# Kernel tuning notes

Measured on AMD Instinct MI355X. Metric: run time of the kernel, lower is better.

The kernel has to match this reference:

```python
import jax, jax.numpy as jnp
import numpy as np

MEM, KEY, VAL, DIN, BS, BQ = 1000, 64, 128, 512, 512, 65536


def setup_inputs() -> dict:
    key = jax.random.key(0)
    ks = jax.random.split(key, 20)

    def lin(k, fan_in, shape):
        return (jax.random.normal(k, shape, jnp.float32) / np.sqrt(fan_in)).astype(jnp.float32)

    return {
        "support_x": jax.random.normal(ks[0], (BS, DIN), jnp.float32),
        "support_y": jax.random.normal(ks[1], (BS, VAL), jnp.float32),
        "query_x": jax.random.normal(ks[2], (BQ, DIN), jnp.float32),
        "query_y": jax.random.normal(ks[3], (BQ, 1), jnp.float32),
        # base model: Linear(DIN -> KEY)
        "base_W": lin(ks[4], DIN, (DIN, KEY)),
        "base_b": jnp.zeros((KEY,), jnp.float32),
        # ExternalMemory projections
        "kp_W": lin(ks[5], KEY, (KEY, KEY)),
        "kp_b": jnp.zeros((KEY,), jnp.float32),
        "vp_W": lin(ks[6], VAL, (VAL, VAL)),
        "vp_b": jnp.zeros((VAL,), jnp.float32),
        # memory buffers (randn keys/values like register_buffer(torch.randn))
        "mem_keys": jax.random.normal(ks[7], (MEM, KEY), jnp.float32),
        "mem_values": jax.random.normal(ks[8], (MEM, VAL), jnp.float32),
        # ages: uniform so top-k picks distinct slots deterministically
        "mem_age": jax.random.uniform(ks[9], (MEM,), jnp.float32),
        # controller MLP: Linear(KEY+VAL,128) ReLU Linear(128,64) ReLU Linear(64,1)
        "c1_W": lin(ks[10], KEY + VAL, (KEY + VAL, 128)),
        "c1_b": jnp.zeros((128,), jnp.float32),
        "c2_W": lin(ks[11], 128, (128, 64)),
        "c2_b": jnp.zeros((64,), jnp.float32),
        "c3_W": lin(ks[12], 64, (64, 1)),
        "c3_b": jnp.zeros((1,), jnp.float32),
    }


def reference(support_x, support_y, query_x, query_y,
              base_W, base_b, kp_W, kp_b, vp_W, vp_b,
              mem_keys, mem_values, mem_age,
              c1_W, c1_b, c2_W, c2_b, c3_W, c3_b):
    # base model features
    support_feat = support_x @ base_W + base_b          # [BS, KEY]
    query_feat = query_x @ base_W + base_b              # [BQ, KEY]

    # --- memory.write(support_feat, support_y) ---
    proj_keys = support_feat @ kp_W + kp_b              # [BS, KEY]
    proj_vals = support_y @ vp_W + vp_b                 # [BS, VAL]
    _, oldest = jax.lax.top_k(mem_age, BS)              # evict oldest BS slots
    new_keys = mem_keys.at[oldest].set(proj_keys)       # [MEM, KEY]
    new_values = mem_values.at[oldest].set(proj_vals)   # [MEM, VAL]

    # --- memory.read(query_feat) ---
    proj_q = query_feat @ kp_W + kp_b                   # [BQ, KEY]
    sims = proj_q @ new_keys.T                          # [BQ, MEM]
    attn = jax.nn.softmax(sims, axis=-1)
    retrieved = attn @ new_values                       # [BQ, VAL]

    # --- controller MLP on [query_feat ; retrieved] ---
    aug = jnp.concatenate([query_feat, retrieved], axis=-1)  # [BQ, KEY+VAL]
    h = jax.nn.relu(aug @ c1_W + c1_b)
    h = jax.nn.relu(h @ c2_W + c2_b)
    query_pred = h @ c3_W + c3_b                        # [BQ, 1]

    meta_loss = jnp.mean((query_pred - query_y) ** 2)
    return meta_loss, query_pred, retrieved
```

## Files before the change

### kernel.cpp

```cpp
#include <hip/hip_runtime.h>

typedef _Float16 h8v __attribute__((ext_vector_type(8)));
typedef _Float16 h4v __attribute__((ext_vector_type(4)));
typedef float    f4v __attribute__((ext_vector_type(4)));

#define MFMA16(a,b,c) __builtin_amdgcn_mfma_f32_16x16x32_f16((a),(b),(c),0,0,0)
#define NEGF (-1e30f)

#define MEM 1000
#define KEY 64
#define VAL 128
#define DIN 512
#define BS  512
#define BQ  65536


typedef __attribute__((address_space(1))) const unsigned int guint;
typedef __attribute__((address_space(3))) unsigned int luint;

__device__ __forceinline__ void gld16(const _Float16* g, _Float16* l)
{
  __builtin_amdgcn_global_load_lds((guint*)g, (luint*)l, 16, 0, 0);
}

__device__ __forceinline__ h8v cvt8(const float* p)
{
  f4v u = *(const f4v*)p;
  f4v v = *(const f4v*)(p + 4);
  h8v a;
  a[0] = (_Float16)u.x; a[1] = (_Float16)u.y; a[2] = (_Float16)u.z; a[3] = (_Float16)u.w;
  a[4] = (_Float16)v.x; a[5] = (_Float16)v.y; a[6] = (_Float16)v.z; a[7] = (_Float16)v.w;
  return a;
}

__device__ __forceinline__ h8v cvt8nt(const float* p)
{
  f4v u = __builtin_nontemporal_load((const f4v*)p);
  f4v v = __builtin_nontemporal_load((const f4v*)(p + 4));
  h8v a;
  a[0] = (_Float16)u.x; a[1] = (_Float16)u.y; a[2] = (_Float16)u.z; a[3] = (_Float16)u.w;
  a[4] = (_Float16)v.x; a[5] = (_Float16)v.y; a[6] = (_Float16)v.z; a[7] = (_Float16)v.w;
  return a;
}

__global__ void k_prep1(const float* __restrict__ baseW, const float* __restrict__ base_b,
                        const float* __restrict__ kpW, const float* __restrict__ kp_b,
                        const float* __restrict__ vpW, const float* __restrict__ c1W,
                        const float* __restrict__ c2W, const float* __restrict__ age,
                        _Float16* __restrict__ WTf, float* __restrict__ bcomb,
                        _Float16* __restrict__ vpWt, _Float16* __restrict__ c1F,
                        _Float16* __restrict__ c2F, int* __restrict__ ranks,
                        float* __restrict__ out0)
{
  long id = (long)blockIdx.x * 256 + threadIdx.x;
  if (id < 65536) {
    int h = (int)id;
    int j = h & 7, lane = (h >> 3) & 63, KS = (h >> 9) & 15, F = h >> 13;
    int n = F * 16 + (lane & 15);
    int k = KS * 32 + ((lane >> 4) << 3) + j;
    float v;
    if (n < 64) v = baseW[(size_t)k * 64 + n];
    else {
      int nn = n - 64;
      const float* br = baseW + (size_t)k * 64;
      float s = 0.f;
      for (int t = 0; t < 64; ++t) s += br[t] * kpW[t * 64 + nn];
      v = s;
    }
    WTf[h] = (_Float16)v;
  } else if (id < 65664) {
    int i = (int)(id - 65536);
    if (i < 64) bcomb[i] = base_b[i];
    else {
      int n = i - 64;
      float s = kp_b[n];
      for (int t = 0; t < 64; ++t) s += base_b[t] * kpW[t * 64 + n];
      bcomb[i] = s;
    }
  } else if (id < 90240) {
    int h = (int)(id - 65664);
    int j = h & 7, lane = (h >> 3) & 63, KS = (h >> 9) % 6, F = (h >> 9) / 6;
    int n = F * 16 + (lane & 15);
    int k = KS * 32 + ((lane >> 4) << 3) + j;
    c1F[h] = (_Float16)c1W[(size_t)k * 128 + n];
  } else if (id < 98432) {
    int h = (int)(id - 90240);
    int j = h & 7, lane = (h >> 3) & 63, KS = (h >> 9) & 3, F = h >> 11;
    int n = F * 16 + (lane & 15);
    int k = KS * 32 + ((lane >> 4) << 3) + j;
    c2F[h] = (_Float16)c2W[(size_t)k * 64 + n];
  } else if (id < 114816) {
    long i = id - 98432;
    int n = (int)(i >> 7), k = (int)(i & 127);
    vpWt[i] = (_Float16)vpW[(size_t)k * 128 + n];
  } else if (id < 115816) {
    int jx = (int)(id - 114816);
    float aj = age[jx];
    int r = 0;
    for (int i2 = 0; i2 < MEM; ++i2) {
      float ai = age[i2];
      r += (ai > aj) || (ai == aj && i2 < jx);
    }
    ranks[jx] = r;
  } else if (id == 115816) {
    *out0 = 0.f;
  }
}

__global__ __launch_bounds__(64) void k_prep2(
    const float* __restrict__ sx, const float* __restrict__ sy,
    const _Float16* __restrict__ WTf, const float* __restrict__ bcomb,
    const _Float16* __restrict__ vpWt, const float* __restrict__ vp_b,
    float* __restrict__ pkeys, float* __restrict__ pvals)
{
  const int lane = threadIdx.x, quad = lane >> 4, l15 = lane & 15;
  const f4v fz = {0.f, 0.f, 0.f, 0.f};
  if (blockIdx.x < 32) {
    const int m0 = blockIdx.x * 16;
    f4v acc[4];
    #pragma unroll
    for (int f = 0; f < 4; ++f) acc[f] = fz;
    const float* xr = sx + (size_t)(m0 + l15) * DIN;
    #pragma unroll 4
    for (int ks = 0; ks < 16; ++ks) {
      int k0 = ks * 32 + quad * 8;
      h8v a = cvt8(xr + k0);
      #pragma unroll
      for (int f = 0; f < 4; ++f) {
        h8v b = *(const h8v*)(WTf + (size_t)((((4 + f) * 16) + ks) * 64 + lane) * 8);
        acc[f] = MFMA16(a, b, acc[f]);
      }
    }
    #pragma unroll
    for (int f = 0; f < 4; ++f) {
      int col = f * 16 + l15;
      float bb = bcomb[64 + col];
      #pragma unroll
      for (int r = 0; r < 4; ++r)
        pkeys[(size_t)(m0 + quad * 4 + r) * KEY + col] = acc[f][r] + bb;
    }
  } else {
    const int m0 = (blockIdx.x - 32) * 16;
    f4v acc[8];
    #pragma unroll
    for (int f = 0; f < 8; ++f) acc[f] = fz;
    const float* yr = sy + (size_t)(m0 + l15) * VAL;
    #pragma unroll
    for (int ks = 0; ks < 4; ++ks) {
      int k0 = ks * 32 + quad * 8;
      h8v a = cvt8(yr + k0);
      #pragma unroll
      for (int f = 0; f < 8; ++f) {
        h8v b = *(const h8v*)(vpWt + (size_t)(f * 16 + l15) * 128 + k0);
        acc[f] = MFMA16(a, b, acc[f]);
      }
    }
    #pragma unroll
    for (int f = 0; f < 8; ++f) {
      int col = f * 16 + l15;
      float bb = vp_b[col];
      #pragma unroll
      for (int r = 0; r < 4; ++r)
        pvals[(size_t)(m0 + quad * 4 + r) * VAL + col] = acc[f][r] + bb;
    }
  }
}

__global__ void k_prep3(const int* __restrict__ ranks, const float* __restrict__ pk,
                        const float* __restrict__ pv, const float* __restrict__ memK,
                        const float* __restrict__ memV,
                        _Float16* __restrict__ keysF, _Float16* __restrict__ valF)
{
  int id = blockIdx.x * 256 + threadIdx.x;
  if (id < 65536) {
    int j = id & 7, lane = (id >> 3) & 63, KS = (id >> 9) & 1, F = id >> 10;
    int n = F * 16 + (lane & 15);
    int k = KS * 32 + ((lane >> 4) << 3) + j;
    float v = 0.f;
    if (n < MEM) {
      int rk = ranks[n];
      v = (rk < BS) ? pk[(size_t)rk * KEY + k] : memK[(size_t)n * KEY + k];
    }
    keysF[id] = (_Float16)v;
  } else {
    int h = id - 65536;
    int j = h & 7, lane = (h >> 3) & 63, KS = (h >> 9) & 31, F = h >> 14;
    int nv = F * 16 + (lane & 15);
    int jm = KS * 32 + ((lane >> 4) << 3) + j;
    float v = 0.f;
    if (jm < MEM) {
      int rk = ranks[jm];
      v = (rk < BS) ? pv[(size_t)rk * VAL + nv] : memV[(size_t)jm * VAL + nv];
    }
    valF[h] = (_Float16)v;
  }
}

__global__ __launch_bounds__(512) void k_feat(const float* __restrict__ qx,
                                              const _Float16* __restrict__ WTf,
                                              const float* __restrict__ bcomb,
                                              _Float16* __restrict__ qfpq)
{
  __shared__ __align__(16) _Float16 WTsh[65536];

  const int tid = threadIdx.x, wid = tid >> 6, lane = tid & 63;
  const int quad = lane >> 4, l15 = lane & 15;

  #pragma unroll
  for (int i = 0; i < 16; ++i) {
    const int t = wid * 16 + i;
    gld16(WTf + (size_t)t * 512 + lane * 8, WTsh + t * 512);
  }
  asm volatile("s_waitcnt vmcnt(0)" ::: "memory");
  __syncthreads();

  const int tile = blockIdx.x * 8 + wid;
  const int q0 = tile * 16;
  const f4v fz = {0.f, 0.f, 0.f, 0.f};
  f4v acc[8];
  #pragma unroll
  for (int f = 0; f < 8; ++f) acc[f] = fz;

  const float* xr = qx + (size_t)(q0 + l15) * DIN;

  #pragma unroll 4
  for (int ks = 0; ks < 16; ++ks) {
    const int k0 = ks * 32 + quad * 8;
    h8v a = cvt8nt(xr + k0);
    #pragma unroll
    for (int f = 0; f < 8; ++f) {
      h8v b = *(const h8v*)(WTsh + (size_t)((f * 16 + ks) * 64 + lane) * 8);
      acc[f] = MFMA16(a, b, acc[f]);
    }
  }

  __syncthreads();
  _Float16* tbuf = WTsh + wid * 2176;

  #pragma unroll
  for (int f = 0; f < 8; ++f) {
    float bb = bcomb[f * 16 + l15];
    #pragma unroll
    for (int r = 0; r < 4; ++r)
      tbuf[(quad * 4 + r) * 136 + f * 16 + l15] = (_Float16)(acc[f][r] + bb);
  }
  const size_t ob = (size_t)tile * 4 * 512;
  #pragma unroll
  for (int KS = 0; KS < 4; ++KS) {
    h8v v = *(const h8v*)&tbuf[l15 * 136 + KS * 32 + quad * 8];
    __builtin_nontemporal_store(v, (h8v*)(qfpq + ob + KS * 512 + lane * 8));
  }
}

__global__ __launch_bounds__(512) void k_main(
    const _Float16* __restrict__ qfpq, const float* __restrict__ qy,
    const float* __restrict__ c1_b, const float* __restrict__ c2_b,
    const float* __restrict__ c3W, const float* __restrict__ c3b,
    const _Float16* __restrict__ c1F, const _Float16* __restrict__ c2F,
    const _Float16* __restrict__ keysF, const _Float16* __restrict__ valF,
    float* __restrict__ dout)
{
  __shared__ __align__(16) _Float16 Ksh[2][8192];
  __shared__ __align__(16) _Float16 Vsh[2][16384];
  __shared__ __align__(16) _Float16 Pwk[8][3328];

  const int tid  = threadIdx.x;
  const int wid  = tid >> 6;
  const int lane = tid & 63;
  const int quad = lane >> 4;
  const int l15  = lane & 15;
  const int tile = blockIdx.x * 8 + wid;
  const int q0   = tile * 16;

  _Float16* P_s  = Pwk[wid];
  _Float16* h2_s = Pwk[wid] + 2176;

  float* out_pred = dout + 1;
  float* out_ret  = dout + 1 + BQ;
  const f4v fz = {0.f, 0.f, 0.f, 0.f};

  {
    const _Float16* kc = keysF;
    #pragma unroll
    for (int i = 0; i < 2; ++i) {
      const int t = wid * 2 + i;
      gld16(kc + (size_t)t * 512 + lane * 8, Ksh[0] + t * 512);
    }
    #pragma unroll
    for (int i = 0; i < 4; ++i) {
      const int t = wid * 4 + i;
      const int v = t >> 2, sub = t & 3;
      gld16(valF + ((size_t)(v * 32 + 0 * 4 + sub)) * 512 + lane * 8,
            Vsh[0] + (v * 4 + sub) * 512);
    }
  }

  const size_t fb = (size_t)tile * 4 * 512;
  h8v pq0 = __builtin_nontemporal_load((const h8v*)(qfpq + fb + 2 * 512 + lane * 8));
  h8v pq1 = __builtin_nontemporal_load((const h8v*)(qfpq + fb + 3 * 512 + lane * 8));

  asm volatile("s_waitcnt vmcnt(0)" ::: "memory");
  __syncthreads();

  float rm[4], rl[4];
  #pragma unroll
  for (int r = 0; r < 4; ++r) { rm[r] = NEGF; rl[r] = 0.f; }
  f4v O[8];
  #pragma unroll
  for (int v = 0; v < 8; ++v) O[v] = fz;

  #pragma unroll 1
  for (int c = 0; c < 8; ++c) {
    const int cur = c & 1;

    if (c < 7) {
      const int nc = c + 1;
      const _Float16* kc = keysF + (size_t)nc * 8192;
      #pragma unroll
      for (int i = 0; i < 2; ++i) {
        const int t = wid * 2 + i;
        gld16(kc + (size_t)t * 512 + lane * 8, Ksh[cur ^ 1] + t * 512);
      }
      #pragma unroll
      for (int i = 0; i < 4; ++i) {
        const int t = wid * 4 + i;
        const int v = t >> 2, sub = t & 3;
        gld16(valF + ((size_t)(v * 32 + nc * 4 + sub)) * 512 + lane * 8,
              Vsh[cur ^ 1] + (v * 4 + sub) * 512);
      }
    }

    f4v S[8];
    #pragma unroll
    for (int f = 0; f < 8; ++f) S[f] = fz;
    const _Float16* Kb = Ksh[cur];
    #pragma unroll
    for (int f = 0; f < 8; ++f) {
      h8v b0 = *(const h8v*)(Kb + (size_t)(f * 2 + 0) * 512 + lane * 8);
      h8v b1 = *(const h8v*)(Kb + (size_t)(f * 2 + 1) * 512 + lane * 8);
      S[f] = MFMA16(pq0, b0, S[f]);
      S[f] = MFMA16(pq1, b1, S[f]);
    }

    float cm[4] = {NEGF, NEGF, NEGF, NEGF};
    #pragma unroll
    for (int f = 0; f < 8; ++f) {
      const int col = c * 128 + f * 16 + l15;
      const bool ok = (col < MEM);
      #pragma unroll
      for (int r = 0; r < 4; ++r) {
        float s = ok ? S[f][r] : NEGF;
        S[f][r] = s;
        cm[r] = fmaxf(cm[r], s);
      }
    }
    #pragma unroll
    for (int r = 0; r < 4; ++r) {
      #pragma unroll
      for (int m = 1; m < 16; m <<= 1) cm[r] = fmaxf(cm[r], __shfl_xor(cm[r], m));
    }
    float al[4];
    #pragma unroll
    for (int r = 0; r < 4; ++r) {
      float mn = fmaxf(rm[r], cm[r]);
      al[r] = __expf(rm[r] - mn);
      rm[r] = mn;
    }
    float psl[4] = {0.f, 0.f, 0.f, 0.f};
    #pragma unroll
    for (int f = 0; f < 8; ++f)
      #pragma unroll
      for (int r = 0; r < 4; ++r) {
        float p = __expf(S[f][r] - rm[r]);
        S[f][r] = p;
        psl[r] += p;
      }
    #pragma unroll
    for (int r = 0; r < 4; ++r) rl[r] = rl[r] * al[r] + psl[r];

    #pragma unroll
    for (int f = 0; f < 8; ++f)
      #pragma unroll
      for (int r = 0; r < 4; ++r)
        P_s[(quad * 4 + r) * 136 + f * 16 + l15] = (_Float16)S[f][r];
    #pragma unroll
    for (int v = 0; v < 8; ++v)
      #pragma unroll
      for (int r = 0; r < 4; ++r) O[v][r] *= al[r];
    const _Float16* Vb = Vsh[cur];
    #pragma unroll
    for (int ks = 0; ks < 4; ++ks) {
      h8v a = *(const h8v*)&P_s[l15 * 136 + ks * 32 + quad * 8];
      #pragma unroll
      for (int v = 0; v < 8; ++v) {
        h8v b = *(const h8v*)(Vb + (size_t)(v * 4 + ks) * 512 + lane * 8);
        O[v] = MFMA16(a, b, O[v]);
      }
    }

    asm volatile("s_waitcnt vmcnt(0)" ::: "memory");
    __syncthreads();
  }

  #pragma unroll
  for (int r = 0; r < 4; ++r) {
    #pragma unroll
    for (int m = 1; m < 16; m <<= 1) rl[r] += __shfl_xor(rl[r], m);
  }

  #pragma unroll
  for (int v = 0; v < 8; ++v)
    #pragma unroll
    for (int r = 0; r < 4; ++r)
      P_s[(quad * 4 + r) * 136 + v * 16 + l15] = (_Float16)(O[v][r] / rl[r]);

  #pragma unroll
  for (int it = 0; it < 8; ++it) {
    int flat = it * 256 + lane * 4;
    int row = flat >> 7, col = flat & 127;
    h4v t = *(const h4v*)&P_s[row * 136 + col];
    f4v o;
    o.x = (float)t[0]; o.y = (float)t[1]; o.z = (float)t[2]; o.w = (float)t[3];
    __builtin_nontemporal_store(o, (f4v*)(out_ret + (size_t)q0 * VAL + flat));
  }

  h8v qf0 = __builtin_nontemporal_load((const h8v*)(qfpq + fb + 0 * 512 + lane * 8));
  h8v qf1 = __builtin_nontemporal_load((const h8v*)(qfpq + fb + 1 * 512 + lane * 8));
  {
    f4v H[8];
    #pragma unroll
    for (int f = 0; f < 8; ++f) H[f] = fz;
    #pragma unroll
    for (int ks = 0; ks < 6; ++ks) {
      const int k0 = ks * 32;
      h8v a = (ks == 0) ? qf0 : (ks == 1) ? qf1
               : *(const h8v*)&P_s[l15 * 136 + (k0 - 64) + quad * 8];
      #pragma unroll
      for (int f = 0; f < 8; ++f) {
        h8v b = *(const h8v*)(c1F + (size_t)(f * 6 + ks) * 512 + lane * 8);
        H[f] = MFMA16(a, b, H[f]);
      }
    }
    #pragma unroll
    for (int f = 0; f < 8; ++f) {
      float bb = c1_b[f * 16 + l15];
      #pragma unroll
      for (int r = 0; r < 4; ++r)
        P_s[(quad * 4 + r) * 136 + f * 16 + l15] =
            (_Float16)fmaxf(0.f, H[f][r] + bb);
    }
  }

  {
    f4v G[4];
    #pragma unroll
    for (int f = 0; f < 4; ++f) G[f] = fz;
    #pragma unroll
    for (int ks = 0; ks < 4; ++ks) {
      h8v a = *(const h8v*)&P_s[l15 * 136 + ks * 32 + quad * 8];
      #pragma unroll
      for (int f = 0; f < 4; ++f) {
        h8v b = *(const h8v*)(c2F + (size_t)(f * 4 + ks) * 512 + lane * 8);
        G[f] = MFMA16(a, b, G[f]);
      }
    }
    #pragma unroll
    for (int f = 0; f < 4; ++f) {
      float bb = c2_b[f * 16 + l15];
      #pragma unroll
      for (int r = 0; r < 4; ++r)
        h2_s[(quad * 4 + r) * 72 + f * 16 + l15] =
            (_Float16)fmaxf(0.f, G[f][r] + bb);
    }
  }

  float lsum;
  {
    const int prow = lane >> 2, pj = lane & 3;
    float s = 0.f;
    #pragma unroll
    for (int k = 0; k < 16; ++k) {
      int kk = pj * 16 + k;
      s += (float)h2_s[prow * 72 + kk] * c3W[kk];
    }
    s += __shfl_xor(s, 1);
    s += __shfl_xor(s, 2);
    float pred = s + c3b[0];
    float diff = pred - qy[q0 + prow];
    if (pj == 0) out_pred[q0 + prow] = pred;
    lsum = diff * diff;
  }
  #pragma unroll
  for (int m = 1; m < 64; m <<= 1) lsum += __shfl_xor(lsum, m);
  if (lane == 0) atomicAdd(dout, lsum * (1.0f / (4.0f * (float)BQ)));
}

extern "C" void kernel_launch(void* const* d_in, const int* in_sizes, int n_in,
                              void* d_out, int out_size, void* d_ws, size_t ws_size,
                              hipStream_t stream)
{
  const float* support_x = (const float*)d_in[0];
  const float* support_y = (const float*)d_in[1];
  const float* query_x   = (const float*)d_in[2];
  const float* query_y   = (const float*)d_in[3];
  const float* base_W    = (const float*)d_in[4];
  const float* base_b    = (const float*)d_in[5];
  const float* kp_W      = (const float*)d_in[6];
  const float* kp_b      = (const float*)d_in[7];
  const float* vp_W      = (const float*)d_in[8];
  const float* vp_b      = (const float*)d_in[9];
  const float* mem_keys  = (const float*)d_in[10];
  const float* mem_vals  = (const float*)d_in[11];
  const float* mem_age   = (const float*)d_in[12];
  const float* c1_W      = (const float*)d_in[13];
  const float* c1_b      = (const float*)d_in[14];
  const float* c2_W      = (const float*)d_in[15];
  const float* c2_b      = (const float*)d_in[16];
  const float* c3_W      = (const float*)d_in[17];
  const float* c3_b      = (const float*)d_in[18];

  char* w = (char*)d_ws;
  _Float16* WTf   = (_Float16*)(w + 0);
  _Float16* vpWt  = (_Float16*)(w + 131072);
  _Float16* c1F   = (_Float16*)(w + 163840);
  _Float16* c2F   = (_Float16*)(w + 212992);
  float*    bcomb = (float*)   (w + 229376);
  int*      ranks = (int*)     (w + 229888);
  float*    pkeys = (float*)   (w + 233984);
  float*    pvals = (float*)   (w + 365056);
  _Float16* keysF = (_Float16*)(w + 627200);
  _Float16* valF  = (_Float16*)(w + 758272);
  _Float16* qfpq  = (_Float16*)(w + 1048576);

  float* out = (float*)d_out;

  hipLaunchKernelGGL(k_prep1, dim3(453), dim3(256), 0, stream,
                     base_W, base_b, kp_W, kp_b, vp_W, c1_W, c2_W, mem_age,
                     WTf, bcomb, vpWt, c1F, c2F, ranks, out);
  hipLaunchKernelGGL(k_prep2, dim3(64), dim3(64), 0, stream,
                     support_x, support_y, WTf, bcomb, vpWt, vp_b, pkeys, pvals);
  hipLaunchKernelGGL(k_prep3, dim3(768), dim3(256), 0, stream,
                     ranks, pkeys, pvals, mem_keys, mem_vals, keysF, valF);
  hipLaunchKernelGGL(k_feat, dim3(BQ / 128), dim3(512), 0, stream,
                     query_x, WTf, bcomb, qfpq);
  hipLaunchKernelGGL(k_main, dim3(BQ / 128), dim3(512), 0, stream,
                     qfpq, query_y, c1_b, c2_b, c3_W, c3_b,
                     c1F, c2F, keysF, valF, out);
}
```

Before: 375.0 us.

## Fuse query feature projection into attention kernel, two tiles per wave

Merges k_feat and k_main into a single kernel, so the fp16 query features and projected queries stay in registers and no longer go through a global workspace. Each wave now handles two 16-row query tiles, so every K/V chunk loaded into LDS is reused twice. The c1 weights are staged into LDS during the last attention chunk. The cost is a 148KB shared-memory block, which limits the kernel to one block per CU despite the launch_bounds hint, plus higher register pressure from the doubled accumulators.

```diff
diff --git a/kernel.cpp b/kernel.cpp
--- a/kernel.cpp
+++ b/kernel.cpp
@@ -196,122 +196,124 @@
   }
 }
 
-__global__ __launch_bounds__(512) void k_feat(const float* __restrict__ qx,
-                                              const _Float16* __restrict__ WTf,
-                                              const float* __restrict__ bcomb,
-                                              _Float16* __restrict__ qfpq)
-{
-  __shared__ __align__(16) _Float16 WTsh[65536];
-
-  const int tid = threadIdx.x, wid = tid >> 6, lane = tid & 63;
-  const int quad = lane >> 4, l15 = lane & 15;
-
-  #pragma unroll
-  for (int i = 0; i < 16; ++i) {
-    const int t = wid * 16 + i;
-    gld16(WTf + (size_t)t * 512 + lane * 8, WTsh + t * 512);
-  }
-  asm volatile("s_waitcnt vmcnt(0)" ::: "memory");
-  __syncthreads();
-
-  const int tile = blockIdx.x * 8 + wid;
-  const int q0 = tile * 16;
-  const f4v fz = {0.f, 0.f, 0.f, 0.f};
-  f4v acc[8];
-  #pragma unroll
-  for (int f = 0; f < 8; ++f) acc[f] = fz;
-
-  const float* xr = qx + (size_t)(q0 + l15) * DIN;
-
-  #pragma unroll 4
-  for (int ks = 0; ks < 16; ++ks) {
-    const int k0 = ks * 32 + quad * 8;
-    h8v a = cvt8nt(xr + k0);
-    #pragma unroll
-    for (int f = 0; f < 8; ++f) {
-      h8v b = *(const h8v*)(WTsh + (size_t)((f * 16 + ks) * 64 + lane) * 8);
-      acc[f] = MFMA16(a, b, acc[f]);
-    }
-  }
-
-  __syncthreads();
-  _Float16* tbuf = WTsh + wid * 2176;
-
-  #pragma unroll
-  for (int f = 0; f < 8; ++f) {
-    float bb = bcomb[f * 16 + l15];
-    #pragma unroll
-    for (int r = 0; r < 4; ++r)
-      tbuf[(quad * 4 + r) * 136 + f * 16 + l15] = (_Float16)(acc[f][r] + bb);
-  }
-  const size_t ob = (size_t)tile * 4 * 512;
-  #pragma unroll
-  for (int KS = 0; KS < 4; ++KS) {
-    h8v v = *(const h8v*)&tbuf[l15 * 136 + KS * 32 + quad * 8];
-    __builtin_nontemporal_store(v, (h8v*)(qfpq + ob + KS * 512 + lane * 8));
-  }
-}
-
-__global__ __launch_bounds__(512) void k_main(
-    const _Float16* __restrict__ qfpq, const float* __restrict__ qy,
+__global__ __launch_bounds__(512, 2) void k_fused(
+    const float* __restrict__ qx, const float* __restrict__ qy,
+    const _Float16* __restrict__ WTf, const float* __restrict__ bcomb,
     const float* __restrict__ c1_b, const float* __restrict__ c2_b,
     const float* __restrict__ c3W, const float* __restrict__ c3b,
     const _Float16* __restrict__ c1F, const _Float16* __restrict__ c2F,
     const _Float16* __restrict__ keysF, const _Float16* __restrict__ valF,
     float* __restrict__ dout)
 {
-  __shared__ __align__(16) _Float16 Ksh[2][8192];
-  __shared__ __align__(16) _Float16 Vsh[2][16384];
-  __shared__ __align__(16) _Float16 Pwk[8][3328];
+  __shared__ __align__(16) char smem[151552];
+  _Float16* const WTsh = (_Float16*)smem;
+  _Float16* const K0   = (_Float16*)smem;
+  _Float16* const K1   = (_Float16*)(smem + 16384);
+  _Float16* const V0   = (_Float16*)(smem + 32768);
+  _Float16* const V1   = (_Float16*)(smem + 65536);
 
   const int tid  = threadIdx.x;
   const int wid  = tid >> 6;
   const int lane = tid & 63;
   const int quad = lane >> 4;
   const int l15  = lane & 15;
-  const int tile = blockIdx.x * 8 + wid;
-  const int q0   = tile * 16;
-
-  _Float16* P_s  = Pwk[wid];
-  _Float16* h2_s = Pwk[wid] + 2176;
+
+  _Float16* const P_s  = (_Float16*)(smem + 98304 + wid * 6656);
+  _Float16* const h2_s = P_s + 2176;
+
+  const int tA  = blockIdx.x * 16 + wid * 2;
+  const int q0A = tA * 16;
+  const int q0B = q0A + 16;
 
   float* out_pred = dout + 1;
   float* out_ret  = dout + 1 + BQ;
   const f4v fz = {0.f, 0.f, 0.f, 0.f};
 
-  {
-    const _Float16* kc = keysF;
-    #pragma unroll
-    for (int i = 0; i < 2; ++i) {
-      const int t = wid * 2 + i;
-      gld16(kc + (size_t)t * 512 + lane * 8, Ksh[0] + t * 512);
-    }
-    #pragma unroll
-    for (int i = 0; i < 4; ++i) {
-      const int t = wid * 4 + i;
-      const int v = t >> 2, sub = t & 3;
-      gld16(valF + ((size_t)(v * 32 + 0 * 4 + sub)) * 512 + lane * 8,
-            Vsh[0] + (v * 4 + sub) * 512);
-    }
-  }
-
-  const size_t fb = (size_t)tile * 4 * 512;
-  h8v pq0 = __builtin_nontemporal_load((const h8v*)(qfpq + fb + 2 * 512 + lane * 8));
-  h8v pq1 = __builtin_nontemporal_load((const h8v*)(qfpq + fb + 3 * 512 + lane * 8));
-
+  #pragma unroll
+  for (int i = 0; i < 16; ++i) {
+    const int t = wid * 16 + i;
+    gld16(WTf + (size_t)t * 512 + lane * 8, WTsh + t * 512);
+  }
   asm volatile("s_waitcnt vmcnt(0)" ::: "memory");
   __syncthreads();
 
-  float rm[4], rl[4];
-  #pragma unroll
-  for (int r = 0; r < 4; ++r) { rm[r] = NEGF; rl[r] = 0.f; }
-  f4v O[8];
-  #pragma unroll
-  for (int v = 0; v < 8; ++v) O[v] = fz;
+  f4v accA[8], accB[8];
+  #pragma unroll
+  for (int f = 0; f < 8; ++f) { accA[f] = fz; accB[f] = fz; }
+  const float* xrA = qx + (size_t)(q0A + l15) * DIN;
+  const float* xrB = qx + (size_t)(q0B + l15) * DIN;
+
+  #pragma unroll 4
+  for (int ks = 0; ks < 16; ++ks) {
+    const int k0 = ks * 32 + quad * 8;
+    h8v aA = cvt8nt(xrA + k0);
+    h8v aB = cvt8nt(xrB + k0);
+    #pragma unroll
+    for (int f = 0; f < 8; ++f) {
+      h8v b = *(const h8v*)(WTsh + (size_t)((f * 16 + ks) * 64 + lane) * 8);
+      accA[f] = MFMA16(aA, b, accA[f]);
+      accB[f] = MFMA16(aB, b, accB[f]);
+    }
+  }
+  __syncthreads();
+
+  _Float16* tbuf = (_Float16*)(smem + wid * 4352);
+  h8v qf0A, qf1A, pq0A, pq1A, qf0B, qf1B, pq0B, pq1B;
+  {
+    #pragma unroll
+    for (int f = 0; f < 8; ++f) {
+      float bb = bcomb[f * 16 + l15];
+      #pragma unroll
+      for (int r = 0; r < 4; ++r)
+        tbuf[(quad * 4 + r) * 136 + f * 16 + l15] = (_Float16)(accA[f][r] + bb);
+    }
+    qf0A = *(const h8v*)&tbuf[l15 * 136 +  0 + quad * 8];
+    qf1A = *(const h8v*)&tbuf[l15 * 136 + 32 + quad * 8];
+    pq0A = *(const h8v*)&tbuf[l15 * 136 + 64 + quad * 8];
+    pq1A = *(const h8v*)&tbuf[l15 * 136 + 96 + quad * 8];
+    #pragma unroll
+    for (int f = 0; f < 8; ++f) {
+      float bb = bcomb[f * 16 + l15];
+      #pragma unroll
+      for (int r = 0; r < 4; ++r)
+        tbuf[(quad * 4 + r) * 136 + f * 16 + l15] = (_Float16)(accB[f][r] + bb);
+    }
+    qf0B = *(const h8v*)&tbuf[l15 * 136 +  0 + quad * 8];
+    qf1B = *(const h8v*)&tbuf[l15 * 136 + 32 + quad * 8];
+    pq0B = *(const h8v*)&tbuf[l15 * 136 + 64 + quad * 8];
+    pq1B = *(const h8v*)&tbuf[l15 * 136 + 96 + quad * 8];
+  }
+  __syncthreads();
+
+  #pragma unroll
+  for (int i = 0; i < 2; ++i) {
+    const int t = wid * 2 + i;
+    gld16(keysF + (size_t)t * 512 + lane * 8, K0 + t * 512);
+  }
+  #pragma unroll
+  for (int i = 0; i < 4; ++i) {
+    const int t = wid * 4 + i;
+    const int v = t >> 2, sub = t & 3;
+    gld16(valF + ((size_t)(v * 32 + sub)) * 512 + lane * 8,
+          V0 + (v * 4 + sub) * 512);
+  }
+  asm volatile("s_waitcnt vmcnt(0)" ::: "memory");
+  __syncthreads();
+
+  float rmA[4], rlA[4], rmB[4], rlB[4];
+  #pragma unroll
+  for (int r = 0; r < 4; ++r) { rmA[r] = NEGF; rlA[r] = 0.f; rmB[r] = NEGF; rlB[r] = 0.f; }
+  f4v OA[8], OB[8];
+  #pragma unroll
+  for (int v = 0; v < 8; ++v) { OA[v] = fz; OB[v] = fz; }
 
   #pragma unroll 1
   for (int c = 0; c < 8; ++c) {
     const int cur = c & 1;
+    _Float16* const Kc = cur ? K1 : K0;
+    _Float16* const Vc = cur ? V1 : V0;
+    _Float16* const Kn = cur ? K0 : K1;
+    _Float16* const Vn = cur ? V0 : V1;
 
     if (c < 7) {
       const int nc = c + 1;
@@ -319,82 +321,96 @@
       #pragma unroll
       for (int i = 0; i < 2; ++i) {
         const int t = wid * 2 + i;
-        gld16(kc + (size_t)t * 512 + lane * 8, Ksh[cur ^ 1] + t * 512);
+        gld16(kc + (size_t)t * 512 + lane * 8, Kn + t * 512);
       }
       #pragma unroll
       for (int i = 0; i < 4; ++i) {
         const int t = wid * 4 + i;
         const int v = t >> 2, sub = t & 3;
         gld16(valF + ((size_t)(v * 32 + nc * 4 + sub)) * 512 + lane * 8,
-              Vsh[cur ^ 1] + (v * 4 + sub) * 512);
-      }
-    }
-
-    f4v S[8];
-    #pragma unroll
-    for (int f = 0; f < 8; ++f) S[f] = fz;
-    const _Float16* Kb = Ksh[cur];
-    #pragma unroll
-    for (int f = 0; f < 8; ++f) {
-      h8v b0 = *(const h8v*)(Kb + (size_t)(f * 2 + 0) * 512 + lane * 8);
-      h8v b1 = *(const h8v*)(Kb + (size_t)(f * 2 + 1) * 512 + lane * 8);
-      S[f] = MFMA16(pq0, b0, S[f]);
-      S[f] = MFMA16(pq1, b1, S[f]);
-    }
-
-    float cm[4] = {NEGF, NEGF, NEGF, NEGF};
-    #pragma unroll
-    for (int f = 0; f < 8; ++f) {
-      const int col = c * 128 + f * 16 + l15;
-      const bool ok = (col < MEM);
+              Vn + (v * 4 + sub) * 512);
+      }
+    } else {
+      #pragma unroll
+      for (int i = 0; i < 6; ++i) {
+        const int t = wid * 6 + i;
+        _Float16* dst = (t < 16) ? (K0 + t * 512) : (V0 + (t - 16) * 512);
+        gld16(c1F + (size_t)t * 512 + lane * 8, dst);
+      }
+    }
+
+    #pragma unroll
+    for (int par = 0; par < 2; ++par) {
+      const h8v p0 = par ? pq0B : pq0A;
+      const h8v p1 = par ? pq1B : pq1A;
+      float* rm = par ? rmB : rmA;
+      float* rl = par ? rlB : rlA;
+      f4v*   O  = par ? OB  : OA;
+
+      f4v S[8];
+      #pragma unroll
+      for (int f = 0; f < 8; ++f) S[f] = fz;
+      #pragma unroll
+      for (int f = 0; f < 8; ++f) {
+        h8v b0 = *(const h8v*)(Kc + (size_t)(f * 2 + 0) * 512 + lane * 8);
+        h8v b1 = *(const h8v*)(Kc + (size_t)(f * 2 + 1) * 512 + lane * 8);
+        S[f] = MFMA16(p0, b0, S[f]);
+        S[f] = MFMA16(p1, b1, S[f]);
+      }
+
+      float cm[4] = {NEGF, NEGF, NEGF, NEGF};
+      #pragma unroll
+      for (int f = 0; f < 8; ++f) {
+        const int col = c * 128 + f * 16 + l15;
+        const bool ok = (col < MEM);
+        #pragma unroll
+        for (int r = 0; r < 4; ++r) {
+          float s = ok ? S[f][r] : NEGF;
+          S[f][r] = s;
+          cm[r] = fmaxf(cm[r], s);
+        }
+      }
       #pragma unroll
       for (int r = 0; r < 4; ++r) {
-        float s = ok ? S[f][r] : NEGF;
-        S[f][r] = s;
-        cm[r] = fmaxf(cm[r], s);
-      }
-    }
-    #pragma unroll
-    for (int r = 0; r < 4; ++r) {
-      #pragma unroll
-      for (int m = 1; m < 16; m <<= 1) cm[r] = fmaxf(cm[r], __shfl_xor(cm[r], m));
-    }
-    float al[4];
-    #pragma unroll
-    for (int r = 0; r < 4; ++r) {
-      float mn = fmaxf(rm[r], cm[r]);
-      al[r] = __expf(rm[r] - mn);
-      rm[r] = mn;
-    }
-    float psl[4] = {0.f, 0.f, 0.f, 0.f};
-    #pragma unroll
-    for (int f = 0; f < 8; ++f)
+        #pragma unroll
+        for (int m = 1; m < 16; m <<= 1) cm[r] = fmaxf(cm[r], __shfl_xor(cm[r], m));
+      }
+      float al[4];
       #pragma unroll
       for (int r = 0; r < 4; ++r) {
-        float p = __expf(S[f][r] - rm[r]);
-        S[f][r] = p;
-        psl[r] += p;
-      }
-    #pragma unroll
-    for (int r = 0; r < 4; ++r) rl[r] = rl[r] * al[r] + psl[r];
-
-    #pragma unroll
-    for (int f = 0; f < 8; ++f)
-      #pragma unroll
-      for (int r = 0; r < 4; ++r)
-        P_s[(quad * 4 + r) * 136 + f * 16 + l15] = (_Float16)S[f][r];
-    #pragma unroll
-    for (int v = 0; v < 8; ++v)
-      #pragma unroll
-      for (int r = 0; r < 4; ++r) O[v][r] *= al[r];
-    const _Float16* Vb = Vsh[cur];
-    #pragma unroll
-    for (int ks = 0; ks < 4; ++ks) {
-      h8v a = *(const h8v*)&P_s[l15 * 136 + ks * 32 + quad * 8];
-      #pragma unroll
-      for (int v = 0; v < 8; ++v) {
-        h8v b = *(const h8v*)(Vb + (size_t)(v * 4 + ks) * 512 + lane * 8);
-        O[v] = MFMA16(a, b, O[v]);
+        float mn = fmaxf(rm[r], cm[r]);
+        al[r] = __expf(rm[r] - mn);
+        rm[r] = mn;
+      }
+      float psl[4] = {0.f, 0.f, 0.f, 0.f};
+      #pragma unroll
+      for (int f = 0; f < 8; ++f)
+        #pragma unroll
+        for (int r = 0; r < 4; ++r) {
+          float p = __expf(S[f][r] - rm[r]);
+          S[f][r] = p;
+          psl[r] += p;
+        }
+      #pragma unroll
+      for (int r = 0; r < 4; ++r) rl[r] = rl[r] * al[r] + psl[r];
+
+      #pragma unroll
+      for (int f = 0; f < 8; ++f)
+        #pragma unroll
+        for (int r = 0; r < 4; ++r)
+          P_s[(quad * 4 + r) * 136 + f * 16 + l15] = (_Float16)S[f][r];
+      #pragma unroll
+      for (int v = 0; v < 8; ++v)
+        #pragma unroll
+        for (int r = 0; r < 4; ++r) O[v][r] *= al[r];
+      #pragma unroll
+      for (int ks = 0; ks < 4; ++ks) {
+        h8v a = *(const h8v*)&P_s[l15 * 136 + ks * 32 + quad * 8];
+        #pragma unroll
+        for (int v = 0; v < 8; ++v) {
+          h8v b = *(const h8v*)(Vc + (size_t)(v * 4 + ks) * 512 + lane * 8);
+          O[v] = MFMA16(a, b, O[v]);
+        }
       }
     }
 
@@ -403,96 +419,106 @@
   }
 
   #pragma unroll
-  for (int r = 0; r < 4; ++r) {
-    #pragma unroll
-    for (int m = 1; m < 16; m <<= 1) rl[r] += __shfl_xor(rl[r], m);
-  }
-
-  #pragma unroll
-  for (int v = 0; v < 8; ++v)
-    #pragma unroll
-    for (int r = 0; r < 4; ++r)
-      P_s[(quad * 4 + r) * 136 + v * 16 + l15] = (_Float16)(O[v][r] / rl[r]);
-
-  #pragma unroll
-  for (int it = 0; it < 8; ++it) {
-    int flat = it * 256 + lane * 4;
-    int row = flat >> 7, col = flat & 127;
-    h4v t = *(const h4v*)&P_s[row * 136 + col];
-    f4v o;
-    o.x = (float)t[0]; o.y = (float)t[1]; o.z = (float)t[2]; o.w = (float)t[3];
-    __builtin_nontemporal_store(o, (f4v*)(out_ret + (size_t)q0 * VAL + flat));
-  }
-
-  h8v qf0 = __builtin_nontemporal_load((const h8v*)(qfpq + fb + 0 * 512 + lane * 8));
-  h8v qf1 = __builtin_nontemporal_load((const h8v*)(qfpq + fb + 1 * 512 + lane * 8));
-  {
-    f4v H[8];
-    #pragma unroll
-    for (int f = 0; f < 8; ++f) H[f] = fz;
-    #pragma unroll
-    for (int ks = 0; ks < 6; ++ks) {
-      const int k0 = ks * 32;
-      h8v a = (ks == 0) ? qf0 : (ks == 1) ? qf1
-               : *(const h8v*)&P_s[l15 * 136 + (k0 - 64) + quad * 8];
+  for (int par = 0; par < 2; ++par) {
+    const int q0 = par ? q0B : q0A;
+    float* rl = par ? rlB : rlA;
+    f4v*   O  = par ? OB  : OA;
+    const h8v qf0 = par ? qf0B : qf0A;
+    const h8v qf1 = par ? qf1B : qf1A;
+
+    #pragma unroll
+    for (int r = 0; r < 4; ++r) {
+      #pragma unroll
+      for (int m = 1; m < 16; m <<= 1) rl[r] += __shfl_xor(rl[r], m);
+    }
+
+    #pragma unroll
+    for (int v = 0; v < 8; ++v)
+      #pragma unroll
+      for (int r = 0; r < 4; ++r)
+        P_s[(quad * 4 + r) * 136 + v * 16 + l15] = (_Float16)(O[v][r] / rl[r]);
+
+    #pragma unroll
+    for (int it = 0; it < 8; ++it) {
+      int flat = it * 256 + lane * 4;
+      int row = flat >> 7, col = flat & 127;
+      h4v t = *(const h4v*)&P_s[row * 136 + col];
+      f4v o;
+      o.x = (float)t[0]; o.y = (float)t[1]; o.z = (float)t[2]; o.w = (float)t[3];
+      __builtin_nontemporal_store(o, (f4v*)(out_ret + (size_t)q0 * VAL + flat));
+    }
+
+    {
+      f4v H[8];
+      #pragma unroll
+      for (int f = 0; f < 8; ++f) H[f] = fz;
+      #pragma unroll
+      for (int ks = 0; ks < 6; ++ks) {
+        const int k0 = ks * 32;
+        h8v a = (ks == 0) ? qf0 : (ks == 1) ? qf1
+                 : *(const h8v*)&P_s[l15 * 136 + (k0 - 64) + quad * 8];
+        #pragma unroll
+        for (int f = 0; f < 8; ++f) {
+          const int t = f * 6 + ks;
+          const _Float16* bp = (t < 16) ? (K0 + (size_t)t * 512)
+                                        : (V0 + (size_t)(t - 16) * 512);
+          h8v b = *(const h8v*)(bp + lane * 8);
+          H[f] = MFMA16(a, b, H[f]);
+        }
+      }
       #pragma unroll
       for (int f = 0; f < 8; ++f) {
-        h8v b = *(const h8v*)(c1F + (size_t)(f * 6 + ks) * 512 + lane * 8);
-        H[f] = MFMA16(a, b, H[f]);
-      }
-    }
-    #pragma unroll
-    for (int f = 0; f < 8; ++f) {
-      float bb = c1_b[f * 16 + l15];
-      #pragma unroll
-      for (int r = 0; r < 4; ++r)
-        P_s[(quad * 4 + r) * 136 + f * 16 + l15] =
-            (_Float16)fmaxf(0.f, H[f][r] + bb);
-    }
-  }
-
-  {
-    f4v G[4];
-    #pragma unroll
-    for (int f = 0; f < 4; ++f) G[f] = fz;
-    #pragma unroll
-    for (int ks = 0; ks < 4; ++ks) {
-      h8v a = *(const h8v*)&P_s[l15 * 136 + ks * 32 + quad * 8];
+        float bb = c1_b[f * 16 + l15];
+        #pragma unroll
+        for (int r = 0; r < 4; ++r)
+          P_s[(quad * 4 + r) * 136 + f * 16 + l15] =
+              (_Float16)fmaxf(0.f, H[f][r] + bb);
+      }
+    }
+
+    {
+      f4v G[4];
+      #pragma unroll
+      for (int f = 0; f < 4; ++f) G[f] = fz;
+      #pragma unroll
+      for (int ks = 0; ks < 4; ++ks) {
+        h8v a = *(const h8v*)&P_s[l15 * 136 + ks * 32 + quad * 8];
+        #pragma unroll
+        for (int f = 0; f < 4; ++f) {
+          h8v b = *(const h8v*)(c2F + (size_t)(f * 4 + ks) * 512 + lane * 8);
+          G[f] = MFMA16(a, b, G[f]);
+        }
+      }
       #pragma unroll
       for (int f = 0; f < 4; ++f) {
-        h8v b = *(const h8v*)(c2F + (size_t)(f * 4 + ks) * 512 + lane * 8);
-        G[f] = MFMA16(a, b, G[f]);
-      }
-    }
-    #pragma unroll
-    for (int f = 0; f < 4; ++f) {
-      float bb = c2_b[f * 16 + l15];
-      #pragma unroll
-      for (int r = 0; r < 4; ++r)
-        h2_s[(quad * 4 + r) * 72 + f * 16 + l15] =
-            (_Float16)fmaxf(0.f, G[f][r] + bb);
-    }
-  }
-
-  float lsum;
-  {
-    const int prow = lane >> 2, pj = lane & 3;
-    float s = 0.f;
-    #pragma unroll
-    for (int k = 0; k < 16; ++k) {
-      int kk = pj * 16 + k;
-      s += (float)h2_s[prow * 72 + kk] * c3W[kk];
-    }
-    s += __shfl_xor(s, 1);
-    s += __shfl_xor(s, 2);
-    float pred = s + c3b[0];
-    float diff = pred - qy[q0 + prow];
-    if (pj == 0) out_pred[q0 + prow] = pred;
-    lsum = diff * diff;
-  }
-  #pragma unroll
-  for (int m = 1; m < 64; m <<= 1) lsum += __shfl_xor(lsum, m);
-  if (lane == 0) atomicAdd(dout, lsum * (1.0f / (4.0f * (float)BQ)));
+        float bb = c2_b[f * 16 + l15];
+        #pragma unroll
+        for (int r = 0; r < 4; ++r)
+          h2_s[(quad * 4 + r) * 72 + f * 16 + l15] =
+              (_Float16)fmaxf(0.f, G[f][r] + bb);
+      }
+    }
+
+    float lsum;
+    {
+      const int prow = lane >> 2, pj = lane & 3;
+      float s = 0.f;
+      #pragma unroll
+      for (int k = 0; k < 16; ++k) {
+        int kk = pj * 16 + k;
+        s += (float)h2_s[prow * 72 + kk] * c3W[kk];
+      }
+      s += __shfl_xor(s, 1);
+      s += __shfl_xor(s, 2);
+      float pred = s + c3b[0];
+      float diff = pred - qy[q0 + prow];
+      if (pj == 0) out_pred[q0 + prow] = pred;
+      lsum = diff * diff;
+    }
+    #pragma unroll
+    for (int m = 1; m < 64; m <<= 1) lsum += __shfl_xor(lsum, m);
+    if (lane == 0) atomicAdd(dout, lsum * (1.0f / (4.0f * (float)BQ)));
+  }
 }
 
 extern "C" void kernel_launch(void* const* d_in, const int* in_sizes, int n_in,
@@ -530,7 +556,6 @@
   float*    pvals = (float*)   (w + 365056);
   _Float16* keysF = (_Float16*)(w + 627200);
   _Float16* valF  = (_Float16*)(w + 758272);
-  _Float16* qfpq  = (_Float16*)(w + 1048576);
 
   float* out = (float*)d_out;
 
@@ -541,9 +566,7 @@
                      support_x, support_y, WTf, bcomb, vpWt, vp_b, pkeys, pvals);
   hipLaunchKernelGGL(k_prep3, dim3(768), dim3(256), 0, stream,
                      ranks, pkeys, pvals, mem_keys, mem_vals, keysF, valF);
-  hipLaunchKernelGGL(k_feat, dim3(BQ / 128), dim3(512), 0, stream,
-                     query_x, WTf, bcomb, qfpq);
-  hipLaunchKernelGGL(k_main, dim3(BQ / 128), dim3(512), 0, stream,
-                     qfpq, query_y, c1_b, c2_b, c3_W, c3_b,
+  hipLaunchKernelGGL(k_fused, dim3(BQ / 256), dim3(512), 0, stream,
+                     query_x, query_y, WTf, bcomb, c1_b, c2_b, c3_W, c3_b,
                      c1F, c2F, keysF, valF, out);
 }
```

New measurement: 377.7 us. About the same (+0.7%).
